# Kernel optimization log

Hardware: AMD Instinct MI355X
Metric: run time of the kernel (lower is better)

The kernel has to match this reference:

```python
import jax, jax.numpy as jnp
import numpy as np
from jax import lax

DIM = 1024
INTER = 512
N_EXPERTS = 16
TOPK = 4
ROUTE_SCALE = 2.5
VOCAB = 32000


def setup_inputs() -> dict:
    key = jax.random.key(0)
    ks = jax.random.split(key, 8)
    x = jax.random.normal(ks[0], (2, 512, DIM), dtype=jnp.float32)
    input_ids = jax.random.randint(ks[1], (2, 512), 0, VOCAB)
    s = 0.02
    gate_w = jax.random.normal(ks[2], (N_EXPERTS, DIM), dtype=jnp.float32) * s
    gate_b = jax.random.normal(ks[3], (N_EXPERTS,), dtype=jnp.float32) * s
    # routed experts: w13 maps dim -> 2*inter (gate|up), w2 maps inter -> dim
    w13 = jax.random.normal(ks[4], (N_EXPERTS, 2 * INTER, DIM), dtype=jnp.float32) * s
    w2 = jax.random.normal(ks[5], (N_EXPERTS, DIM, INTER), dtype=jnp.float32) * s
    # shared expert
    w13_s = jax.random.normal(ks[6], (2 * INTER, DIM), dtype=jnp.float32) * s
    w2_s = jax.random.normal(ks[7], (DIM, INTER), dtype=jnp.float32) * s
    return {"x": x, "input_ids": input_ids, "gate_w": gate_w, "gate_b": gate_b,
            "w13": w13, "w2": w2, "w13_s": w13_s, "w2_s": w2_s}


def _silu_and_mul(gu):
    gate, up = jnp.split(gu, 2, axis=-1)
    return jax.nn.silu(gate) * up


def reference(x, input_ids, gate_w, gate_b, w13, w2, w13_s, w2_s):
    B, S, D = x.shape
    xt = x.reshape(-1, D)                      # [T, D]
    T = xt.shape[0]
    # ---- Gate (sigmoid score func, bias added for selection only) ----
    scores = jax.nn.sigmoid(xt.astype(jnp.float32) @ gate_w.T)   # [T, E]
    biased = scores + gate_b
    _, idx = lax.top_k(biased, TOPK)                             # [T, K] int
    w = jnp.take_along_axis(scores, idx, axis=-1)                # [T, K]
    w = w / jnp.sum(w, axis=-1, keepdims=True)                   # normalize (non-softmax)
    w = w * ROUTE_SCALE
    # ---- dispatch/combine as dense per-expert combine weights ----
    comb = jnp.zeros((T, N_EXPERTS), jnp.float32)
    comb = comb.at[jnp.arange(T)[:, None], idx].add(w)           # [T, E]
    comb = comb.astype(x.dtype)

    def expert_body(y, args):
        w13_e, w2_e, c_e = args                                  # [2I,D], [D,I], [T]
        h = _silu_and_mul(xt @ w13_e.T)                          # [T, I]
        return y + c_e[:, None] * (h @ w2_e.T), None

    y, _ = lax.scan(expert_body, jnp.zeros_like(xt), (w13, w2, comb.T))
    # ---- shared expert ----
    y = y + _silu_and_mul(xt @ w13_s.T) @ w2_s.T
    return y.astype(x.dtype).reshape(B, S, D)
```

## Files before the change

kernel.cpp:

```cpp
#include <hip/hip_runtime.h>
#include <hip/hip_bf16.h>
#include <math.h>

#define NTOK   1024
#define DIMX   1024
#define INTERX 512
#define NEXP   16
#define RSCALE 2.5f

typedef _Float16 f16x8 __attribute__((ext_vector_type(8)));
typedef float    f32x4 __attribute__((ext_vector_type(4)));

#define N_W13  (NEXP * 2 * INTERX * DIMX)
#define N_W2   (NEXP * DIMX * INTERX)
#define N_W13S (2 * INTERX * DIMX)
#define N_W2S  (DIMX * INTERX)
#define N_X    (NTOK * DIMX)
#define N_CVT  ((size_t)N_W13 + N_W2 + N_W13S + N_W2S + N_X)

#define WS_COUNTS  0
#define WS_TOKIDX  256
#define WS_SLOTS   (WS_TOKIDX + NEXP * NTOK * 4)
#define WS_WQ      (WS_SLOTS + NTOK * 16)
#define WS_SEL     (WS_WQ + NTOK * 16)
#define WS_H       (WS_SEL + NTOK * 16)
#define WS_YC      (WS_H + (size_t)5120 * 512 * 2)
#define WS_F16     (WS_YC + (size_t)5120 * 1024 * 4)
#define WS_NEED    (WS_F16 + N_CVT * 2)

#define SWZ(r, k) ((r) * 64 + ((k) ^ (((r) & 7) << 3)))

#define CVT_BLOCKS 3392

__device__ __forceinline__ f16x8 ldcvt(const float* __restrict__ p) {
    const float4 a = *(const float4*)p;
    const float4 b = *(const float4*)(p + 4);
    return (f16x8){(_Float16)a.x, (_Float16)a.y, (_Float16)a.z, (_Float16)a.w,
                   (_Float16)b.x, (_Float16)b.y, (_Float16)b.z, (_Float16)b.w};
}

__device__ __forceinline__ void gl_lds16(const _Float16* g, _Float16* l) {
    __builtin_amdgcn_global_load_lds(
        (const __attribute__((address_space(1))) void*)g,
        (__attribute__((address_space(3))) void*)l, 16, 0, 0);
}

__device__ __forceinline__ void unswz1088(int L, int& mt, int& y, int& e) {
    const int xcd = L & 7;
    const int k   = L >> 3;
    const int panel = xcd * 17 + (k >> 3);
    mt = k & 7;
    e  = panel >> 3;
    y  = panel & 7;
}

__global__ __launch_bounds__(256) void cvt_all(
    const float* __restrict__ w13, const float* __restrict__ w2,
    const float* __restrict__ w13s, const float* __restrict__ w2s,
    const float* __restrict__ x, _Float16* __restrict__ dh)
{
    const size_t base8 = (size_t)blockIdx.x * 256 + threadIdx.x;
#pragma unroll
    for (int it = 0; it < 4; ++it) {
        const size_t i8 = base8 + (size_t)it * (CVT_BLOCKS * 256);
        size_t off = i8 * 8;
        const float* s;
        if (off < N_W13)                       s = w13 + off;
        else if ((off -= N_W13) < N_W2)        s = w2 + off;
        else if ((off -= N_W2) < N_W13S)       s = w13s + off;
        else if ((off -= N_W13S) < N_W2S)      s = w2s + off;
        else                                   s = x + (off - N_W2S);
        *(f16x8*)(dh + i8 * 8) = ldcvt(s);
    }
}

__global__ __launch_bounds__(256) void gate(
    const float* __restrict__ x, const float* __restrict__ gw,
    const float* __restrict__ gb,
    int* __restrict__ sel, float* __restrict__ wq)
{
    const int t    = blockIdx.x * 4 + (threadIdx.x >> 6);
    const int lane = threadIdx.x & 63;
    const int e    = lane & 15;
    const int q    = lane >> 4;

    const float4* xq = (const float4*)(x + (size_t)t * DIMX) + q * 64;
    const float4* gq = (const float4*)(gw + (size_t)e * DIMX) + q * 64;
    float s0 = 0.f, s1 = 0.f, s2 = 0.f, s3 = 0.f;
#pragma unroll 8
    for (int i = 0; i < 64; i += 2) {
        const float4 a = xq[i],     b = gq[i];
        const float4 c = xq[i + 1], d = gq[i + 1];
        s0 = fmaf(a.x, b.x, s0); s1 = fmaf(a.y, b.y, s1);
        s2 = fmaf(a.z, b.z, s2); s3 = fmaf(a.w, b.w, s3);
        s0 = fmaf(c.x, d.x, s0); s1 = fmaf(c.y, d.y, s1);
        s2 = fmaf(c.z, d.z, s2); s3 = fmaf(c.w, d.w, s3);
    }
    float acc = (s0 + s1) + (s2 + s3);
    acc += __shfl_xor(acc, 16);
    acc += __shfl_xor(acc, 32);

    const float sv = 1.f / (1.f + __expf(-acc));
    float v = (lane < 16) ? (sv + gb[e]) : -1e30f;

    float wk0, wk1, wk2, wk3; int ek0, ek1, ek2, ek3;
    float wsum = 0.f;
#pragma unroll
    for (int k = 0; k < 4; ++k) {
        float bestv = v; int besti = lane;
#pragma unroll
        for (int off = 8; off >= 1; off >>= 1) {
            const float ov = __shfl_xor(bestv, off);
            const int   oi = __shfl_xor(besti, off);
            if (ov > bestv || (ov == bestv && oi < besti)) { bestv = ov; besti = oi; }
        }
        besti = __shfl(besti, 0);
        const float sbest = __shfl(sv, besti);
        if (k == 0) { wk0 = sbest; ek0 = besti; }
        if (k == 1) { wk1 = sbest; ek1 = besti; }
        if (k == 2) { wk2 = sbest; ek2 = besti; }
        if (k == 3) { wk3 = sbest; ek3 = besti; }
        wsum += sbest;
        if (lane == besti) v = -1e30f;
    }
    const float scale = RSCALE / wsum;

    if (lane == 0) {
        sel[t * 4 + 0] = ek0;  wq[t * 4 + 0] = wk0 * scale;
        sel[t * 4 + 1] = ek1;  wq[t * 4 + 1] = wk1 * scale;
        sel[t * 4 + 2] = ek2;  wq[t * 4 + 2] = wk2 * scale;
        sel[t * 4 + 3] = ek3;  wq[t * 4 + 3] = wk3 * scale;
    }
}

__global__ __launch_bounds__(1024) void build(
    const int* __restrict__ sel,
    int* __restrict__ counts, int* __restrict__ tok_idx,
    int* __restrict__ slots)
{
    __shared__ int lc[NEXP];
    const int t = threadIdx.x;
    if (t < NEXP) lc[t] = 0;
    __syncthreads();

    int e0 = sel[t * 4 + 0], e1 = sel[t * 4 + 1];
    int e2 = sel[t * 4 + 2], e3 = sel[t * 4 + 3];
    int p0 = atomicAdd(&lc[e0], 1);
    int p1 = atomicAdd(&lc[e1], 1);
    int p2 = atomicAdd(&lc[e2], 1);
    int p3 = atomicAdd(&lc[e3], 1);
    tok_idx[e0 * NTOK + p0] = t;  slots[t * 4 + 0] = (e0 << 10) | p0;
    tok_idx[e1 * NTOK + p1] = t;  slots[t * 4 + 1] = (e1 << 10) | p1;
    tok_idx[e2 * NTOK + p2] = t;  slots[t * 4 + 2] = (e2 << 10) | p2;
    tok_idx[e3 * NTOK + p3] = t;  slots[t * 4 + 3] = (e3 << 10) | p3;

    __syncthreads();
    if (t < NEXP) counts[t] = lc[t];
}

__global__ __launch_bounds__(256, 2) void ffn1g(
    const _Float16* __restrict__ xh,
    const _Float16* __restrict__ w13h, const _Float16* __restrict__ w13sh,
    const int* __restrict__ counts, const int* __restrict__ tok_idx,
    _Float16* __restrict__ h)
{
    int mt, y, e;
    unswz1088(blockIdx.x, mt, y, e);
    const int Me = (e == NEXP) ? NTOK : counts[e];
    const int m0 = mt * 128;
    if (m0 >= Me) return;
    const int g0 = y * 64;
    int rowbase = 0;
    if (e == NEXP) rowbase = 4096;
    else for (int i = 0; i < e; ++i) rowbase += counts[i];

    const int tid = threadIdx.x, lane = tid & 63;
    const int wid = tid >> 6;
    const int wm = wid >> 1, wn = wid & 1;
    const int li = lane & 15, rk = (lane >> 4) * 8;

    const _Float16* Wh = (e == NEXP) ? w13sh : (w13h + (size_t)e * (2 * INTERX) * DIMX);

    __shared__ _Float16 T[2][256 * 64];

    const int lrow = lane >> 3;
    const int lc   = (lane & 7) ^ lrow;
    const _Float16* src[8];
    int ldsoff[8];
#pragma unroll
    for (int j = 0; j < 8; ++j) {
        const int c = wid * 8 + j;
        const int r = c * 8 + lrow;
        ldsoff[j] = c * 512;
        if (r < 128) {
            int ma = m0 + r; if (ma >= Me) ma = Me - 1;
            const int tok = (e == NEXP) ? ma : tok_idx[e * NTOK + ma];
            src[j] = xh + (size_t)tok * DIMX + lc * 8;
        } else {
            const int rb = r - 128;
            const int bwn = rb >> 6, bf = (rb >> 4) & 3, bli = rb & 15;
            const int wrow = ((bf & 2) ? INTERX : 0) + g0 + bwn * 32 + (bf & 1) * 16 + bli;
            src[j] = Wh + (size_t)wrow * DIMX + lc * 8;
        }
    }

    f32x4 acc[4][4];
#pragma unroll
    for (int i = 0; i < 4; ++i)
#pragma unroll
        for (int f = 0; f < 4; ++f) acc[i][f] = (f32x4){0.f, 0.f, 0.f, 0.f};

    auto STAGE = [&](int b, int k0) {
#pragma unroll
        for (int j = 0; j < 8; ++j)
            gl_lds16(src[j] + k0, &T[b][ldsoff[j]]);
    };
    auto MM = [&](int b) {
#pragma unroll
        for (int kk = 0; kk < 64; kk += 32) {
            f16x8 afr[4], bfr[4];
#pragma unroll
            for (int i = 0; i < 4; ++i) {
                const int r = wm * 64 + i * 16 + li;
                afr[i] = *(const f16x8*)&T[b][SWZ(r, kk + rk)];
            }
#pragma unroll
            for (int f = 0; f < 4; ++f) {
                const int r = 128 + wn * 64 + f * 16 + li;
                bfr[f] = *(const f16x8*)&T[b][SWZ(r, kk + rk)];
            }
#pragma unroll
            for (int i = 0; i < 4; ++i)
#pragma unroll
                for (int f = 0; f < 4; ++f)
                    acc[i][f] = __builtin_amdgcn_mfma_f32_16x16x32_f16(
                        afr[i], bfr[f], acc[i][f], 0, 0, 0);
        }
    };

    STAGE(0, 0);
    __syncthreads();
    int cur = 0;
#pragma unroll
    for (int t = 0; t < DIMX / 64; ++t) {
        if (t + 1 < DIMX / 64) STAGE(cur ^ 1, (t + 1) * 64);
        MM(cur);
        __syncthreads();
        cur ^= 1;
    }

#pragma unroll
    for (int i = 0; i < 4; ++i) {
#pragma unroll
        for (int q = 0; q < 4; ++q) {
            const int m = m0 + wm * 64 + i * 16 + (lane >> 4) * 4 + q;
            if (m >= Me) continue;
            _Float16* hp = h + (size_t)(rowbase + m) * INTERX + g0 + wn * 32 + li;
#pragma unroll
            for (int f = 0; f < 2; ++f) {
                const float g = acc[i][f][q];
                const float u = acc[i][f + 2][q];
                hp[f * 16] = (_Float16)(g * u / (1.f + __expf(-g)));
            }
        }
    }
}

__global__ __launch_bounds__(256, 2) void ffn2g(
    const _Float16* __restrict__ w2h, const _Float16* __restrict__ w2sh,
    const int* __restrict__ counts, const _Float16* __restrict__ h,
    float* __restrict__ yc)
{
    int mt, y, e;
    unswz1088(blockIdx.x, mt, y, e);
    const int Me = (e == NEXP) ? NTOK : counts[e];
    const int m0 = mt * 128;
    if (m0 >= Me) return;
    const int n0 = y * 128;
    int rowbase = 0;
    if (e == NEXP) rowbase = 4096;
    else for (int i = 0; i < e; ++i) rowbase += counts[i];

    const int tid = threadIdx.x, lane = tid & 63;
    const int wid = tid >> 6;
    const int wm = wid >> 1, wn = wid & 1;
    const int li = lane & 15, rk = (lane >> 4) * 8;

    const _Float16* Wh = (e == NEXP) ? w2sh : (w2h + (size_t)e * DIMX * INTERX);

    __shared__ _Float16 T[2][256 * 64];

    const int lrow = lane >> 3;
    const int lc   = (lane & 7) ^ lrow;
    const _Float16* src[8];
    int ldsoff[8];
#pragma unroll
    for (int j = 0; j < 8; ++j) {
        const int c = wid * 8 + j;
        const int r = c * 8 + lrow;
        ldsoff[j] = c * 512;
        if (r < 128) {
            src[j] = h + (size_t)(rowbase + m0 + r) * INTERX + lc * 8;
        } else {
            const int rb = r - 128;
            src[j] = Wh + (size_t)(n0 + rb) * INTERX + lc * 8;
        }
    }

    f32x4 acc[4][4];
#pragma unroll
    for (int i = 0; i < 4; ++i)
#pragma unroll
        for (int f = 0; f < 4; ++f) acc[i][f] = (f32x4){0.f, 0.f, 0.f, 0.f};

    auto STAGE = [&](int b, int k0) {
#pragma unroll
        for (int j = 0; j < 8; ++j)
            gl_lds16(src[j] + k0, &T[b][ldsoff[j]]);
    };
    auto MM = [&](int b) {
#pragma unroll
        for (int kk = 0; kk < 64; kk += 32) {
            f16x8 afr[4], bfr[4];
#pragma unroll
            for (int i = 0; i < 4; ++i) {
                const int r = wm * 64 + i * 16 + li;
                afr[i] = *(const f16x8*)&T[b][SWZ(r, kk + rk)];
            }
#pragma unroll
            for (int f = 0; f < 4; ++f) {
                const int r = 128 + wn * 64 + f * 16 + li;
                bfr[f] = *(const f16x8*)&T[b][SWZ(r, kk + rk)];
            }
#pragma unroll
            for (int i = 0; i < 4; ++i)
#pragma unroll
                for (int f = 0; f < 4; ++f)
                    acc[i][f] = __builtin_amdgcn_mfma_f32_16x16x32_f16(
                        afr[i], bfr[f], acc[i][f], 0, 0, 0);
        }
    };

    STAGE(0, 0);
    __syncthreads();
    int cur = 0;
#pragma unroll
    for (int t = 0; t < INTERX / 64; ++t) {
        if (t + 1 < INTERX / 64) STAGE(cur ^ 1, (t + 1) * 64);
        MM(cur);
        __syncthreads();
        cur ^= 1;
    }

#pragma unroll
    for (int i = 0; i < 4; ++i) {
#pragma unroll
        for (int q = 0; q < 4; ++q) {
            const int m = m0 + wm * 64 + i * 16 + (lane >> 4) * 4 + q;
            if (m >= Me) continue;
            float* yp = yc + (size_t)(rowbase + m) * DIMX + n0 + wn * 64 + li;
#pragma unroll
            for (int f = 0; f < 4; ++f)
                yp[f * 16] = acc[i][f][q];
        }
    }
}

struct Stage { f16x8 a0, a1, b0, b1, b2, b3; };

__global__ __launch_bounds__(256, 3) void ffn1f(
    const float* __restrict__ xf,
    const float* __restrict__ w13f, const float* __restrict__ w13sf,
    const int* __restrict__ counts, const int* __restrict__ tok_idx,
    _Float16* __restrict__ h)
{
    const int e  = blockIdx.z;
    const int Me = (e == NEXP) ? NTOK : counts[e];
    const int m0 = blockIdx.x * 64;
    if (m0 >= Me) return;
    const int g0 = blockIdx.y * 64;
    int rowbase = 0;
    if (e == NEXP) rowbase = 4096;
    else for (int i = 0; i < e; ++i) rowbase += counts[i];

    const int tid = threadIdx.x, lane = tid & 63;
    const int wm = tid >> 7, wn = (tid >> 6) & 1;
    const int li = lane & 15, rk = (lane >> 4) * 8;
    const int sr = tid >> 3;
    const int sc = (tid & 7) * 8;

    int ma0 = m0 + sr;      if (ma0 >= Me) ma0 = Me - 1;
    int ma1 = m0 + sr + 32; if (ma1 >= Me) ma1 = Me - 1;
    const int tok0 = (e == NEXP) ? ma0 : tok_idx[e * NTOK + ma0];
    const int tok1 = (e == NEXP) ? ma1 : tok_idx[e * NTOK + ma1];

    size_t boff[4];
#pragma unroll
    for (int j = 0; j < 4; ++j) {
        const int c = sr + 32 * j;
        const int bwn = c >> 6, bf = (c >> 4) & 3, bli = c & 15;
        const int row = ((bf & 2) ? INTERX : 0) + g0 + bwn * 32 + (bf & 1) * 16 + bli;
        boff[j] = (size_t)row * DIMX + sc;
    }
    const float* Wf = (e == NEXP) ? w13sf : (w13f + (size_t)e * (2 * INTERX) * DIMX);
    const size_t aoff0 = (size_t)tok0 * DIMX + sc;
    const size_t aoff1 = (size_t)tok1 * DIMX + sc;

    __shared__ _Float16 As[2][64 * 64];
    __shared__ _Float16 Bs[2][128 * 64];

    f32x4 acc[2][4];
#pragma unroll
    for (int i = 0; i < 2; ++i)
#pragma unroll
        for (int f = 0; f < 4; ++f) acc[i][f] = (f32x4){0.f, 0.f, 0.f, 0.f};

    auto LD = [&](int k) -> Stage {
        Stage st;
        st.a0 = ldcvt(xf + aoff0 + k);
        st.a1 = ldcvt(xf + aoff1 + k);
        st.b0 = ldcvt(Wf + boff[0] + k);
        st.b1 = ldcvt(Wf + boff[1] + k);
        st.b2 = ldcvt(Wf + boff[2] + k);
        st.b3 = ldcvt(Wf + boff[3] + k);
        return st;
    };
    auto WRb = [&](int b, const Stage& st) {
        *(f16x8*)&As[b][SWZ(sr, sc)]      = st.a0;
        *(f16x8*)&As[b][SWZ(sr + 32, sc)] = st.a1;
        *(f16x8*)&Bs[b][SWZ(sr, sc)]      = st.b0;
        *(f16x8*)&Bs[b][SWZ(sr + 32, sc)] = st.b1;
        *(f16x8*)&Bs[b][SWZ(sr + 64, sc)] = st.b2;
        *(f16x8*)&Bs[b][SWZ(sr + 96, sc)] = st.b3;
    };
    auto MM = [&](int b) {
#pragma unroll
        for (int kk = 0; kk < 64; kk += 32) {
            f16x8 afr[2], bfr[4];
#pragma unroll
            for (int i = 0; i < 2; ++i)
                afr[i] = *(const f16x8*)&As[b][SWZ(wm * 32 + i * 16 + li, kk + rk)];
#pragma unroll
            for (int f = 0; f < 4; ++f)
                bfr[f] = *(const f16x8*)&Bs[b][SWZ(wn * 64 + f * 16 + li, kk + rk)];
#pragma unroll
            for (int i = 0; i < 2; ++i)
#pragma unroll
                for (int f = 0; f < 4; ++f)
                    acc[i][f] = __builtin_amdgcn_mfma_f32_16x16x32_f16(
                        afr[i], bfr[f], acc[i][f], 0, 0, 0);
        }
    };

    Stage rB = LD(0);
    WRb(0, rB);
    rB = LD(64);
    Stage rC = LD(128);
#pragma unroll
    for (int t = 0; t < DIMX / 64; ++t) {
        __syncthreads();
        Stage rN;
        if (t + 3 < DIMX / 64) rN = LD((t + 3) * 64); else rN = rC;
        MM(t & 1);
        WRb((t & 1) ^ 1, rB);
        rB = rC; rC = rN;
    }

#pragma unroll
    for (int i = 0; i < 2; ++i) {
#pragma unroll
        for (int q = 0; q < 4; ++q) {
            const int m = m0 + wm * 32 + i * 16 + (lane >> 4) * 4 + q;
            if (m >= Me) continue;
            _Float16* hp = h + (size_t)(rowbase + m) * INTERX + g0 + wn * 32 + li;
#pragma unroll
            for (int f = 0; f < 2; ++f) {
                const float g = acc[i][f][q];
                const float u = acc[i][f + 2][q];
                hp[f * 16] = (_Float16)(g * u / (1.f + __expf(-g)));
            }
        }
    }
}

__global__ __launch_bounds__(256, 3) void ffn2f(
    const float* __restrict__ w2f, const float* __restrict__ w2sf,
    const int* __restrict__ counts, const _Float16* __restrict__ h,
    float* __restrict__ yc)
{
    const int e  = blockIdx.z;
    const int Me = (e == NEXP) ? NTOK : counts[e];
    const int m0 = blockIdx.x * 64;
    if (m0 >= Me) return;
    const int n0 = blockIdx.y * 128;
    int rowbase = 0;
    if (e == NEXP) rowbase = 4096;
    else for (int i = 0; i < e; ++i) rowbase += counts[i];

    const int tid = threadIdx.x, lane = tid & 63;
    const int wm = tid >> 7, wn = (tid >> 6) & 1;
    const int li = lane & 15, rk = (lane >> 4) * 8;
    const int sr = tid >> 3;
    const int sc = (tid & 7) * 8;

    const _Float16* pA0 = h + (size_t)(rowbase + m0 + sr) * INTERX + sc;
    const _Float16* pA1 = pA0 + (size_t)32 * INTERX;
    const float* Wf = (e == NEXP) ? w2sf : (w2f + (size_t)e * DIMX * INTERX);
    size_t boff[4];
#pragma unroll
    for (int j = 0; j < 4; ++j) boff[j] = (size_t)(n0 + sr + 32 * j) * INTERX + sc;

    __shared__ _Float16 As[2][64 * 64];
    __shared__ _Float16 Bs[2][128 * 64];

    f32x4 acc[2][4];
#pragma unroll
    for (int i = 0; i < 2; ++i)
#pragma unroll
        for (int f = 0; f < 4; ++f) acc[i][f] = (f32x4){0.f, 0.f, 0.f, 0.f};

    auto LD = [&](int k) -> Stage {
        Stage st;
        st.a0 = *(const f16x8*)(pA0 + k);
        st.a1 = *(const f16x8*)(pA1 + k);
        st.b0 = ldcvt(Wf + boff[0] + k);
        st.b1 = ldcvt(Wf + boff[1] + k);
        st.b2 = ldcvt(Wf + boff[2] + k);
        st.b3 = ldcvt(Wf + boff[3] + k);
        return st;
    };
    auto WRb = [&](int b, const Stage& st) {
        *(f16x8*)&As[b][SWZ(sr, sc)]      = st.a0;
        *(f16x8*)&As[b][SWZ(sr + 32, sc)] = st.a1;
        *(f16x8*)&Bs[b][SWZ(sr, sc)]      = st.b0;
        *(f16x8*)&Bs[b][SWZ(sr + 32, sc)] = st.b1;
        *(f16x8*)&Bs[b][SWZ(sr + 64, sc)] = st.b2;
        *(f16x8*)&Bs[b][SWZ(sr + 96, sc)] = st.b3;
    };
    auto MM = [&](int b) {
#pragma unroll
        for (int kk = 0; kk < 64; kk += 32) {
            f16x8 afr[2], bfr[4];
#pragma unroll
            for (int i = 0; i < 2; ++i)
                afr[i] = *(const f16x8*)&As[b][SWZ(wm * 32 + i * 16 + li, kk + rk)];
#pragma unroll
            for (int f = 0; f < 4; ++f)
                bfr[f] = *(const f16x8*)&Bs[b][SWZ(wn * 64 + f * 16 + li, kk + rk)];
#pragma unroll
            for (int i = 0; i < 2; ++i)
#pragma unroll
                for (int f = 0; f < 4; ++f)
                    acc[i][f] = __builtin_amdgcn_mfma_f32_16x16x32_f16(
                        afr[i], bfr[f], acc[i][f], 0, 0, 0);
        }
    };

    Stage rB = LD(0);
    WRb(0, rB);
    rB = LD(64);
    Stage rC = LD(128);
#pragma unroll
    for (int t = 0; t < INTERX / 64; ++t) {
        __syncthreads();
        Stage rN;
        if (t + 3 < INTERX / 64) rN = LD((t + 3) * 64); else rN = rC;
        MM(t & 1);
        WRb((t & 1) ^ 1, rB);
        rB = rC; rC = rN;
    }

#pragma unroll
    for (int i = 0; i < 2; ++i) {
#pragma unroll
        for (int q = 0; q < 4; ++q) {
            const int m = m0 + wm * 32 + i * 16 + (lane >> 4) * 4 + q;
            if (m >= Me) continue;
            float* yp = yc + (size_t)(rowbase + m) * DIMX + n0 + wn * 64 + li;
#pragma unroll
            for (int f = 0; f < 4; ++f)
                yp[f * 16] = acc[i][f][q];
        }
    }
}

__global__ __launch_bounds__(256) void combine(
    const int* __restrict__ counts,
    const int* __restrict__ slots,
    const float* __restrict__ wq,
    const float* __restrict__ yc,
    float* __restrict__ out)
{
    __shared__ int soff[NEXP];
    if (threadIdx.x < NEXP) {
        int o = 0;
        for (int i = 0; i < (int)threadIdx.x; ++i) o += counts[i];
        soff[threadIdx.x] = o;
    }
    __syncthreads();

    const int t = blockIdx.x;
    const int tid = threadIdx.x;
    const float4* ycv = (const float4*)yc;
    float4 a = ycv[(size_t)(4096 + t) * 256 + tid];
#pragma unroll
    for (int k = 0; k < 4; ++k) {
        const int s   = slots[t * 4 + k];
        const int e   = s >> 10, pos = s & 1023;
        const float w = wq[t * 4 + k];
        const float4 v = ycv[(size_t)(soff[e] + pos) * 256 + tid];
        a.x = fmaf(w, v.x, a.x); a.y = fmaf(w, v.y, a.y);
        a.z = fmaf(w, v.z, a.z); a.w = fmaf(w, v.w, a.w);
    }
    ((float4*)out)[(size_t)t * 256 + tid] = a;
}

extern "C" void kernel_launch(void* const* d_in, const int* in_sizes, int n_in,
                              void* d_out, int out_size, void* d_ws, size_t ws_size,
                              hipStream_t stream)
{
    const float* x    = (const float*)d_in[0];
    const float* gw   = (const float*)d_in[2];
    const float* gb   = (const float*)d_in[3];
    const float* w13  = (const float*)d_in[4];
    const float* w2   = (const float*)d_in[5];
    const float* w13s = (const float*)d_in[6];
    const float* w2s  = (const float*)d_in[7];
    float* out = (float*)d_out;

    char* ws = (char*)d_ws;
    int*       counts  = (int*)(ws + WS_COUNTS);
    int*       tok_idx = (int*)(ws + WS_TOKIDX);
    int*       slots   = (int*)(ws + WS_SLOTS);
    float*     wq      = (float*)(ws + WS_WQ);
    int*       sel     = (int*)(ws + WS_SEL);
    _Float16*  h       = (_Float16*)(ws + WS_H);
    float*     yc      = (float*)(ws + WS_YC);
    _Float16*  dh      = (_Float16*)(ws + WS_F16);
    _Float16*  w13h    = dh;
    _Float16*  w2h     = w13h + N_W13;
    _Float16*  w13sh   = w2h + N_W2;
    _Float16*  w2sh    = w13sh + N_W13S;
    _Float16*  xh      = w2sh + N_W2S;

    const bool F16 = (ws_size >= WS_NEED);

    gate<<<NTOK / 4, 256, 0, stream>>>(x, gw, gb, sel, wq);
    build<<<1, 1024, 0, stream>>>(sel, counts, tok_idx, slots);
    if (F16)
        cvt_all<<<CVT_BLOCKS, 256, 0, stream>>>(w13, w2, w13s, w2s, x, dh);

    if (F16) {
        ffn1g<<<1088, 256, 0, stream>>>(xh, w13h, w13sh, counts, tok_idx, h);
        ffn2g<<<1088, 256, 0, stream>>>(w2h, w2sh, counts, h, yc);
    } else {
        dim3 g1(16, 8, 17), g2(16, 8, 17);
        ffn1f<<<g1, 256, 0, stream>>>(x, w13, w13s, counts, tok_idx, h);
        ffn2f<<<g2, 256, 0, stream>>>(w2, w2s, counts, h, yc);
    }
    combine<<<NTOK, 256, 0, stream>>>(counts, slots, wq, yc, out);
}
```

Baseline: 98.43 us.

## Compact MoE tile list in build kernel and use explicit vmcnt waits

The build kernel now emits a compacted list of (expert, m0, row offset) tiles, so the FFN kernels index live tiles directly instead of decoding a fixed 1088-block XCD-swizzled grid and exiting early on empty tiles. This removes the per-block prefix sum over counts and packs active blocks at the front of the grid, at the cost of dropping the XCD-aware panel swizzle. The GEMM main loops also replace __syncthreads with explicit s_waitcnt vmcnt plus raw barriers, so the next stage's async loads can stay in flight while the current stage computes. The extra barrier per iteration and the loss of L2 locality from the swizzle could offset the gain.

```diff
diff --git a/kernel.cpp b/kernel.cpp
--- a/kernel.cpp
+++ b/kernel.cpp
@@ -23,7 +23,11 @@
 #define WS_SLOTS   (WS_TOKIDX + NEXP * NTOK * 4)
 #define WS_WQ      (WS_SLOTS + NTOK * 16)
 #define WS_SEL     (WS_WQ + NTOK * 16)
-#define WS_H       (WS_SEL + NTOK * 16)
+#define WS_NT      (WS_SEL + NTOK * 16)
+#define WS_TE      (WS_NT + 64)
+#define WS_TM      (WS_TE + 1024)
+#define WS_TR      (WS_TM + 1024)
+#define WS_H       (WS_TR + 1024)
 #define WS_YC      (WS_H + (size_t)5120 * 512 * 2)
 #define WS_F16     (WS_YC + (size_t)5120 * 1024 * 4)
 #define WS_NEED    (WS_F16 + N_CVT * 2)
@@ -43,15 +47,6 @@
     __builtin_amdgcn_global_load_lds(
         (const __attribute__((address_space(1))) void*)g,
         (__attribute__((address_space(3))) void*)l, 16, 0, 0);
-}
-
-__device__ __forceinline__ void unswz1088(int L, int& mt, int& y, int& e) {
-    const int xcd = L & 7;
-    const int k   = L >> 3;
-    const int panel = xcd * 17 + (k >> 3);
-    mt = k & 7;
-    e  = panel >> 3;
-    y  = panel & 7;
 }
 
 __global__ __launch_bounds__(256) void cvt_all(
@@ -136,7 +131,9 @@
 __global__ __launch_bounds__(1024) void build(
     const int* __restrict__ sel,
     int* __restrict__ counts, int* __restrict__ tok_idx,
-    int* __restrict__ slots)
+    int* __restrict__ slots,
+    int* __restrict__ n_tiles, int* __restrict__ tile_e,
+    int* __restrict__ tile_m0, int* __restrict__ tile_r0)
 {
     __shared__ int lc[NEXP];
     const int t = threadIdx.x;
@@ -156,23 +153,45 @@
 
     __syncthreads();
     if (t < NEXP) counts[t] = lc[t];
-}
+    if (t == 0) {
+        int nt = 0, row = 0;
+        for (int e = 0; e <= NEXP; ++e) {
+            const int c = (e == NEXP) ? NTOK : lc[e];
+            for (int m0 = 0; m0 < c; m0 += 128) {
+                tile_e[nt]  = e;
+                tile_m0[nt] = m0;
+                tile_r0[nt] = row + m0;
+                ++nt;
+            }
+            row += c;
+        }
+        n_tiles[0] = nt;
+    }
+}
+
+#define WAITV8()  do { asm volatile("s_waitcnt vmcnt(8)" ::: "memory"); \
+                       __builtin_amdgcn_sched_barrier(0); } while (0)
+#define WAITV0()  do { asm volatile("s_waitcnt vmcnt(0)" ::: "memory"); \
+                       __builtin_amdgcn_sched_barrier(0); } while (0)
+#define RBAR()    do { __builtin_amdgcn_s_barrier(); \
+                       __builtin_amdgcn_sched_barrier(0); } while (0)
 
 __global__ __launch_bounds__(256, 2) void ffn1g(
     const _Float16* __restrict__ xh,
     const _Float16* __restrict__ w13h, const _Float16* __restrict__ w13sh,
     const int* __restrict__ counts, const int* __restrict__ tok_idx,
+    const int* __restrict__ n_tiles, const int* __restrict__ tile_e,
+    const int* __restrict__ tile_m0, const int* __restrict__ tile_r0,
     _Float16* __restrict__ h)
 {
-    int mt, y, e;
-    unswz1088(blockIdx.x, mt, y, e);
+    const int tile = blockIdx.x >> 3;
+    if (tile >= n_tiles[0]) return;
+    const int y  = blockIdx.x & 7;
+    const int e  = tile_e[tile];
+    const int m0 = tile_m0[tile];
+    const int rowbase = tile_r0[tile] - m0;
     const int Me = (e == NEXP) ? NTOK : counts[e];
-    const int m0 = mt * 128;
-    if (m0 >= Me) return;
     const int g0 = y * 64;
-    int rowbase = 0;
-    if (e == NEXP) rowbase = 4096;
-    else for (int i = 0; i < e; ++i) rowbase += counts[i];
 
     const int tid = threadIdx.x, lane = tid & 63;
     const int wid = tid >> 6;
@@ -239,13 +258,20 @@
     };
 
     STAGE(0, 0);
-    __syncthreads();
+    WAITV0();
+    RBAR();
     int cur = 0;
 #pragma unroll
     for (int t = 0; t < DIMX / 64; ++t) {
-        if (t + 1 < DIMX / 64) STAGE(cur ^ 1, (t + 1) * 64);
+        if (t + 1 < DIMX / 64) {
+            STAGE(cur ^ 1, (t + 1) * 64);
+            WAITV8();
+        } else {
+            WAITV0();
+        }
+        RBAR();
         MM(cur);
-        __syncthreads();
+        RBAR();
         cur ^= 1;
     }
 
@@ -269,17 +295,18 @@
 __global__ __launch_bounds__(256, 2) void ffn2g(
     const _Float16* __restrict__ w2h, const _Float16* __restrict__ w2sh,
     const int* __restrict__ counts, const _Float16* __restrict__ h,
+    const int* __restrict__ n_tiles, const int* __restrict__ tile_e,
+    const int* __restrict__ tile_m0, const int* __restrict__ tile_r0,
     float* __restrict__ yc)
 {
-    int mt, y, e;
-    unswz1088(blockIdx.x, mt, y, e);
+    const int tile = blockIdx.x >> 3;
+    if (tile >= n_tiles[0]) return;
+    const int y  = blockIdx.x & 7;
+    const int e  = tile_e[tile];
+    const int m0 = tile_m0[tile];
+    const int rowbase = tile_r0[tile] - m0;
     const int Me = (e == NEXP) ? NTOK : counts[e];
-    const int m0 = mt * 128;
-    if (m0 >= Me) return;
     const int n0 = y * 128;
-    int rowbase = 0;
-    if (e == NEXP) rowbase = 4096;
-    else for (int i = 0; i < e; ++i) rowbase += counts[i];
 
     const int tid = threadIdx.x, lane = tid & 63;
     const int wid = tid >> 6;
@@ -342,13 +369,20 @@
     };
 
     STAGE(0, 0);
-    __syncthreads();
+    WAITV0();
+    RBAR();
     int cur = 0;
 #pragma unroll
     for (int t = 0; t < INTERX / 64; ++t) {
-        if (t + 1 < INTERX / 64) STAGE(cur ^ 1, (t + 1) * 64);
+        if (t + 1 < INTERX / 64) {
+            STAGE(cur ^ 1, (t + 1) * 64);
+            WAITV8();
+        } else {
+            WAITV0();
+        }
+        RBAR();
         MM(cur);
-        __syncthreads();
+        RBAR();
         cur ^= 1;
     }
 
@@ -634,6 +668,10 @@
     int*       slots   = (int*)(ws + WS_SLOTS);
     float*     wq      = (float*)(ws + WS_WQ);
     int*       sel     = (int*)(ws + WS_SEL);
+    int*       n_tiles = (int*)(ws + WS_NT);
+    int*       tile_e  = (int*)(ws + WS_TE);
+    int*       tile_m0 = (int*)(ws + WS_TM);
+    int*       tile_r0 = (int*)(ws + WS_TR);
     _Float16*  h       = (_Float16*)(ws + WS_H);
     float*     yc      = (float*)(ws + WS_YC);
     _Float16*  dh      = (_Float16*)(ws + WS_F16);
@@ -646,13 +684,16 @@
     const bool F16 = (ws_size >= WS_NEED);
 
     gate<<<NTOK / 4, 256, 0, stream>>>(x, gw, gb, sel, wq);
-    build<<<1, 1024, 0, stream>>>(sel, counts, tok_idx, slots);
+    build<<<1, 1024, 0, stream>>>(sel, counts, tok_idx, slots,
+                                  n_tiles, tile_e, tile_m0, tile_r0);
     if (F16)
         cvt_all<<<CVT_BLOCKS, 256, 0, stream>>>(w13, w2, w13s, w2s, x, dh);
 
     if (F16) {
-        ffn1g<<<1088, 256, 0, stream>>>(xh, w13h, w13sh, counts, tok_idx, h);
-        ffn2g<<<1088, 256, 0, stream>>>(w2h, w2sh, counts, h, yc);
+        ffn1g<<<1088, 256, 0, stream>>>(xh, w13h, w13sh, counts, tok_idx,
+                                        n_tiles, tile_e, tile_m0, tile_r0, h);
+        ffn2g<<<1088, 256, 0, stream>>>(w2h, w2sh, counts, h,
+                                        n_tiles, tile_e, tile_m0, tile_r0, yc);
     } else {
         dim3 g1(16, 8, 17), g2(16, 8, 17);
         ffn1f<<<g1, 256, 0, stream>>>(x, w13, w13s, counts, tok_idx, h);
```

Result: faster. 94.11 us (-4.4%).
